# Performance work log

Hardware: AMD Instinct MI355X
Metric: run time of the kernel (lower is better)

## Reference

```python
import jax, jax.numpy as jnp
import numpy as np


def setup_inputs() -> dict:
    key = jax.random.key(0)
    k1, k2 = jax.random.split(key)
    B, S_ENC, S_DEC, D = 8, 2048, 2048, 1024
    enc_outputs = jax.random.normal(k1, (B, S_ENC, D), dtype=jnp.float32)
    dec_outputs = jax.random.normal(k2, (B, S_DEC, D), dtype=jnp.float32)
    return {"enc_outputs": enc_outputs, "dec_outputs": dec_outputs}


def reference(enc_outputs, dec_outputs):
    # scores: [B, S_enc, S_dec] = enc @ dec^T (unscaled)
    a_t = jnp.einsum('bed,btd->bet', enc_outputs, dec_outputs)
    a_t = jax.nn.softmax(a_t, axis=-1)
    # context: [B, S_dec, D] = a_t^T @ enc
    c_t = jnp.einsum('bet,bed->btd', a_t, enc_outputs)
    return c_t
```

## Files before the change

### kernel.cpp

```cpp
#include <hip/hip_runtime.h>


typedef _Float16 half8 __attribute__((ext_vector_type(8)));
typedef _Float16 half4v __attribute__((ext_vector_type(4)));
typedef float floatx16 __attribute__((ext_vector_type(16)));

#define BM 128
#define BN 128
#define BK 64

__device__ __forceinline__ void async_load16(const _Float16* g, void* l) {
  __builtin_amdgcn_global_load_lds(
      (const __attribute__((address_space(1))) void*)g,
      (__attribute__((address_space(3))) void*)l, 16, 0, 0);
}

template <typename OutT, bool TRANS, int RN>
__global__ __launch_bounds__(256, 2) void gemm_bt(
    const _Float16* __restrict__ A, const _Float16* __restrict__ Bt,
    OutT* __restrict__ C, int K, long strideA, long strideB, long strideC,
    int ldA, int ldB, int ldC) {
  constexpr int CPR = BK / 8;
  constexpr int SK = BK / 16;
  __shared__ alignas(16) char smem[TRANS ? (128 * 136 * 2) : (2 * BM * BK * 2)];
  _Float16* lds_a = (_Float16*)smem;
  _Float16* lds_b = (_Float16*)(smem + BM * BK * 2);

  const int b = blockIdx.z;
  A += (long)b * strideA;
  Bt += (long)b * strideB;
  C += (long)b * strideC;

  const int id = blockIdx.y * gridDim.x + blockIdx.x;
  const int xcd = id & 7;
  const int l = id >> 3;
  const int m0 = ((xcd & 3) * 4 + l / RN) * BM;
  const int n0 = ((xcd >> 2) * RN + l % RN) * BN;

  const int tid = threadIdx.x;
  const int lane = tid & 63;
  const int wave = tid >> 6;
  const int l31 = lane & 31;
  const int kh = lane >> 5;
  const int wm = (wave >> 1) * 64;
  const int wn = (wave & 1) * 64;

  floatx16 acc[2][2] = {};

  for (int k0 = 0; k0 < K; k0 += BK) {
#pragma unroll
    for (int c = 0; c < 4; ++c) {
      const int off = c * 4096 + wave * 1024 + lane * 16;
      const int row = off >> 7;
      const int ke = (((off >> 4) & (CPR - 1)) ^ (row & (CPR - 1))) * 8;
      async_load16(A + (long)(m0 + row) * ldA + k0 + ke, (char*)lds_a + off);
      async_load16(Bt + (long)(n0 + row) * ldB + k0 + ke, (char*)lds_b + off);
    }
    __syncthreads();

    half8 af[2][SK], bf[2][SK];
#pragma unroll
    for (int i = 0; i < 2; ++i) {
      const int ra = wm + i * 32 + l31;
      const int rb = wn + i * 32 + l31;
#pragma unroll
      for (int s = 0; s < SK; ++s) {
        const int ck = s * 2 + kh;
        af[i][s] = *(const half8*)((const char*)lds_a + ra * (BK * 2) +
                                   ((ck ^ (ra & (CPR - 1))) << 4));
        bf[i][s] = *(const half8*)((const char*)lds_b + rb * (BK * 2) +
                                   ((ck ^ (rb & (CPR - 1))) << 4));
      }
    }
#pragma unroll
    for (int s = 0; s < SK; ++s)
#pragma unroll
      for (int i = 0; i < 2; ++i)
#pragma unroll
        for (int j = 0; j < 2; ++j)
          acc[i][j] = __builtin_amdgcn_mfma_f32_32x32x16_f16(
              af[i][s], bf[j][s], acc[i][j], 0, 0, 0);
    __syncthreads();
  }

  if constexpr (TRANS) {
    _Float16(*TT)[136] = (_Float16(*)[136])smem;
#pragma unroll
    for (int i = 0; i < 2; ++i)
#pragma unroll
      for (int j = 0; j < 2; ++j) {
        const int tl = wn + j * 32 + l31;
#pragma unroll
        for (int g = 0; g < 4; ++g) {
          half4v h;
#pragma unroll
          for (int rr = 0; rr < 4; ++rr) h[rr] = (_Float16)acc[i][j][g * 4 + rr];
          *(half4v*)&TT[tl][wm + i * 32 + 4 * kh + g * 8] = h;
        }
      }
    __syncthreads();
#pragma unroll
    for (int p = 0; p < 8; ++p) {
      const int idx = p * 256 + tid;
      const int tl = idx >> 4;
      const int ck = idx & 15;
      *(half8*)((_Float16*)C + (long)(n0 + tl) * ldC + m0 + ck * 8) =
          *(const half8*)&TT[tl][ck * 8];
    }
  } else {
#pragma unroll
    for (int i = 0; i < 2; ++i) {
      const int r_base = m0 + wm + i * 32 + 4 * kh;
#pragma unroll
      for (int j = 0; j < 2; ++j) {
        const int col = n0 + wn + j * 32 + l31;
#pragma unroll
        for (int g = 0; g < 4; ++g)
#pragma unroll
          for (int rr = 0; rr < 4; ++rr)
            C[(long)(r_base + g * 8 + rr) * ldC + col] =
                (OutT)acc[i][j][g * 4 + rr];
      }
    }
  }
}

__global__ __launch_bounds__(256) void conv_enc(const float* __restrict__ E,
                                                _Float16* __restrict__ Eh,
                                                _Float16* __restrict__ EhT,
                                                int Se, int D) {
  __shared__ _Float16 T[64][72];
  const int b = blockIdx.z;
  const int d0 = blockIdx.x * 64;
  const int e0 = blockIdx.y * 64;
  const float* Eb = E + (size_t)b * Se * D;
  _Float16* Ehb = Eh + (size_t)b * Se * D;
  _Float16* EhTb = EhT + (size_t)b * D * Se;
  const int tid = threadIdx.x;
  const int tx = tid & 15;
  const int ty = tid >> 4;

  half4v h[4];
#pragma unroll
  for (int r = 0; r < 4; ++r) {
    const int e = e0 + ty * 4 + r;
    float4 v = *(const float4*)(Eb + (size_t)e * D + d0 + tx * 4);
    h[r][0] = (_Float16)v.x; h[r][1] = (_Float16)v.y;
    h[r][2] = (_Float16)v.z; h[r][3] = (_Float16)v.w;
    *(half4v*)(Ehb + (size_t)e * D + d0 + tx * 4) = h[r];
  }
#pragma unroll
  for (int c = 0; c < 4; ++c) {
    half4v w;
#pragma unroll
    for (int r = 0; r < 4; ++r) w[r] = h[r][c];
    *(half4v*)&T[tx * 4 + c][ty * 4] = w;
  }
  __syncthreads();
#pragma unroll
  for (int p = 0; p < 2; ++p) {
    const int idx = tid + p * 256;
    const int row = idx >> 3;
    const int ck = idx & 7;
    *(half8*)(EhTb + (size_t)(d0 + row) * Se + e0 + ck * 8) =
        *(const half8*)&T[row][ck * 8];
  }
}

__global__ __launch_bounds__(256) void conv_dec(const float* __restrict__ X,
                                                _Float16* __restrict__ Y) {
  const size_t i = ((size_t)blockIdx.x * 256 + threadIdx.x) * 8;
  float4 a = *(const float4*)(X + i);
  float4 b = *(const float4*)(X + i + 4);
  half8 h;
  h[0] = (_Float16)a.x; h[1] = (_Float16)a.y;
  h[2] = (_Float16)a.z; h[3] = (_Float16)a.w;
  h[4] = (_Float16)b.x; h[5] = (_Float16)b.y;
  h[6] = (_Float16)b.z; h[7] = (_Float16)b.w;
  *(half8*)(Y + i) = h;
}

__global__ __launch_bounds__(256) void col_stats(const _Float16* __restrict__ ST,
                                                 float2* __restrict__ part) {
  __shared__ float2 red[16][65];
  const int b = blockIdx.z;
  const int e0 = blockIdx.x * 64;
  const int t0 = blockIdx.y * 512;
  const _Float16* S = ST + (size_t)b * 2048 * 2048;
  const int tx = threadIdx.x & 15;
  const int ty = threadIdx.x >> 4;

  float m[4] = {-1e30f, -1e30f, -1e30f, -1e30f};
  float s[4] = {0.f, 0.f, 0.f, 0.f};
  for (int it = 0; it < 32; ++it) {
    const int t = t0 + it * 16 + ty;
    half4v v = *(const half4v*)(S + (size_t)t * 2048 + e0 + tx * 4);
#pragma unroll
    for (int c = 0; c < 4; ++c) {
      const float x = (float)v[c];
      const float m2 = fmaxf(m[c], x);
      s[c] = s[c] * __expf(m[c] - m2) + __expf(x - m2);
      m[c] = m2;
    }
  }
#pragma unroll
  for (int c = 0; c < 4; ++c) red[ty][tx * 4 + c] = make_float2(m[c], s[c]);
  __syncthreads();
  if (threadIdx.x < 64) {
    float2 a = red[0][threadIdx.x];
#pragma unroll
    for (int r = 1; r < 16; ++r) {
      const float2 o = red[r][threadIdx.x];
      const float m2 = fmaxf(a.x, o.x);
      a.y = a.y * __expf(a.x - m2) + o.y * __expf(o.x - m2);
      a.x = m2;
    }
    part[(size_t)blockIdx.y * 16384 + (size_t)b * 2048 + e0 + threadIdx.x] = a;
  }
}

__global__ __launch_bounds__(256) void stats_combine(
    const float2* __restrict__ part, float2* __restrict__ stats) {
  const int idx = blockIdx.x * 256 + threadIdx.x;
  float2 a = part[idx];
#pragma unroll
  for (int tc = 1; tc < 4; ++tc) {
    const float2 o = part[tc * 16384 + idx];
    const float m2 = fmaxf(a.x, o.x);
    a.y = a.y * __expf(a.x - m2) + o.y * __expf(o.x - m2);
    a.x = m2;
  }
  stats[idx] = make_float2(a.x, 1.0f / a.y);
}

__global__ __launch_bounds__(256) void norm_stream(
    const _Float16* __restrict__ ST, const float2* __restrict__ stats,
    _Float16* __restrict__ P) {
  const int b = blockIdx.y;
  const int t0 = blockIdx.x * 4;
  const int e = threadIdx.x * 8;
  float m_[8], rl_[8];
#pragma unroll
  for (int j = 0; j < 8; ++j) {
    const float2 st = stats[(size_t)b * 2048 + e + j];
    m_[j] = st.x;
    rl_[j] = st.y;
  }
  const size_t base = ((size_t)b * 2048 + t0) * 2048 + e;
#pragma unroll
  for (int r = 0; r < 4; ++r) {
    half8 v = *(const half8*)(ST + base + (size_t)r * 2048);
    half8 o;
#pragma unroll
    for (int j = 0; j < 8; ++j)
      o[j] = (_Float16)(__expf((float)v[j] - m_[j]) * rl_[j]);
    *(half8*)(P + base + (size_t)r * 2048) = o;
  }
}

extern "C" void kernel_launch(void* const* d_in, const int* in_sizes, int n_in,
                              void* d_out, int out_size, void* d_ws,
                              size_t ws_size, hipStream_t stream) {
  const float* enc = (const float*)d_in[0];
  const float* dec = (const float*)d_in[1];
  float* out = (float*)d_out;

  const int B = 8, SE = 2048, SD = 2048, D = 1024;
  char* ws = (char*)d_ws;
  _Float16* enc_h = (_Float16*)ws;
  _Float16* dec_h = (_Float16*)(ws + 33554432);
  _Float16* P = (_Float16*)ws;
  _Float16* enc_hT = (_Float16*)(ws + 67108864);
  _Float16* ST = (_Float16*)(ws + 100663296);
  float2* stats = (float2*)(ws + 167772160);
  float2* part = (float2*)(ws + 167903232);

  conv_enc<<<dim3(D / 64, SE / 64, B), 256, 0, stream>>>(enc, enc_h, enc_hT,
                                                         SE, D);
  conv_dec<<<dim3((size_t)B * SD * D / 2048), 256, 0, stream>>>(dec, dec_h);
  gemm_bt<_Float16, true, 8><<<dim3(SD / BN, SE / BM, B), 256, 0, stream>>>(
      enc_h, dec_h, ST, D, (long)SE * D, (long)SD * D, (long)SE * SD, D, D,
      SE);
  col_stats<<<dim3(32, 4, B), 256, 0, stream>>>(ST, part);
  stats_combine<<<dim3(64), 256, 0, stream>>>(part, stats);
  norm_stream<<<dim3(512, B), 256, 0, stream>>>(ST, stats, P);
  gemm_bt<float, false, 4><<<dim3(D / BN, SD / BM, B), 256, 0, stream>>>(
      P, enc_hT, out, SE, (long)SD * SE, (long)D * SE, (long)SD * D, SE, SE,
      D);
}
```

Measured before the change: 364.9 us.

## Replace GEMM with 256x256 double-buffered 8-wave pipelined MFMA kernel

Replaces the 128x128 single-stage GEMM with a 256x256 tile kernel using 512 threads, 128KB of dynamic LDS with double buffering, and 16x16x32 MFMAs interleaved with async global-to-LDS loads. Barriers, priority hints and vmcnt waits are placed by hand. The score GEMM now computes the transposed layout directly by swapping its operands, which drops the LDS transpose epilogue. The aim is to hide load latency and raise arithmetic intensity per tile. In exchange, occupancy falls and the epilogue's stores are scalar and strided.

```diff
diff --git a/kernel.cpp b/kernel.cpp
--- a/kernel.cpp
+++ b/kernel.cpp
@@ -3,11 +3,7 @@
 
 typedef _Float16 half8 __attribute__((ext_vector_type(8)));
 typedef _Float16 half4v __attribute__((ext_vector_type(4)));
-typedef float floatx16 __attribute__((ext_vector_type(16)));
-
-#define BM 128
-#define BN 128
-#define BK 64
+typedef float floatx4 __attribute__((ext_vector_type(4)));
 
 __device__ __forceinline__ void async_load16(const _Float16* g, void* l) {
   __builtin_amdgcn_global_load_lds(
@@ -15,112 +11,150 @@
       (__attribute__((address_space(3))) void*)l, 16, 0, 0);
 }
 
-template <typename OutT, bool TRANS, int RN>
-__global__ __launch_bounds__(256, 2) void gemm_bt(
+template <typename OutT>
+__global__ __launch_bounds__(512, 2) void gemm8p(
     const _Float16* __restrict__ A, const _Float16* __restrict__ Bt,
     OutT* __restrict__ C, int K, long strideA, long strideB, long strideC,
     int ldA, int ldB, int ldC) {
-  constexpr int CPR = BK / 8;
-  constexpr int SK = BK / 16;
-  __shared__ alignas(16) char smem[TRANS ? (128 * 136 * 2) : (2 * BM * BK * 2)];
-  _Float16* lds_a = (_Float16*)smem;
-  _Float16* lds_b = (_Float16*)(smem + BM * BK * 2);
-
-  const int b = blockIdx.z;
-  A += (long)b * strideA;
-  Bt += (long)b * strideB;
-  C += (long)b * strideC;
-
-  const int id = blockIdx.y * gridDim.x + blockIdx.x;
-  const int xcd = id & 7;
-  const int l = id >> 3;
-  const int m0 = ((xcd & 3) * 4 + l / RN) * BM;
-  const int n0 = ((xcd >> 2) * RN + l % RN) * BN;
-
+  extern __shared__ char smem_[];
   const int tid = threadIdx.x;
   const int lane = tid & 63;
   const int wave = tid >> 6;
-  const int l31 = lane & 31;
-  const int kh = lane >> 5;
-  const int wm = (wave >> 1) * 64;
-  const int wn = (wave & 1) * 64;
-
-  floatx16 acc[2][2] = {};
-
-  for (int k0 = 0; k0 < K; k0 += BK) {
-#pragma unroll
-    for (int c = 0; c < 4; ++c) {
-      const int off = c * 4096 + wave * 1024 + lane * 16;
+  const int wm = wave >> 2;
+  const int wn = wave & 3;
+  const int l15 = lane & 15;
+  const int lh = lane >> 4;
+
+  const int gx = gridDim.x, gxy = gridDim.x * gridDim.y;
+  int fid = blockIdx.z * gxy + blockIdx.y * gx + blockIdx.x;
+  const int nwg = gxy * gridDim.z;
+  fid = (fid & 7) * (nwg >> 3) + (fid >> 3);
+  const int b = fid / gxy;
+  const int rem = fid - b * gxy;
+  const int m0 = (rem / gx) * 256;
+  const int n0 = (rem % gx) * 256;
+
+  A += (long)b * strideA + (long)m0 * ldA;
+  Bt += (long)b * strideB + (long)n0 * ldB;
+  C += (long)b * strideC;
+
+  floatx4 acc[8][4] = {};
+  half8 a[4][2], b0[2][2], b1[2][2];
+
+  auto stage = [&](const _Float16* g, int ld, int k0, char* slot) {
+#pragma unroll
+    for (int i = 0; i < 4; ++i) {
+      const int off = i * 8192 + tid * 16;
       const int row = off >> 7;
-      const int ke = (((off >> 4) & (CPR - 1)) ^ (row & (CPR - 1))) * 8;
-      async_load16(A + (long)(m0 + row) * ldA + k0 + ke, (char*)lds_a + off);
-      async_load16(Bt + (long)(n0 + row) * ldB + k0 + ke, (char*)lds_b + off);
+      const int ck = (off >> 4) & 7;
+      async_load16(g + (long)row * ld + k0 + ((ck ^ (row & 7)) << 3),
+                   slot + off);
     }
-    __syncthreads();
-
-    half8 af[2][SK], bf[2][SK];
-#pragma unroll
-    for (int i = 0; i < 2; ++i) {
-      const int ra = wm + i * 32 + l31;
-      const int rb = wn + i * 32 + l31;
-#pragma unroll
-      for (int s = 0; s < SK; ++s) {
-        const int ck = s * 2 + kh;
-        af[i][s] = *(const half8*)((const char*)lds_a + ra * (BK * 2) +
-                                   ((ck ^ (ra & (CPR - 1))) << 4));
-        bf[i][s] = *(const half8*)((const char*)lds_b + rb * (BK * 2) +
-                                   ((ck ^ (rb & (CPR - 1))) << 4));
-      }
-    }
-#pragma unroll
-    for (int s = 0; s < SK; ++s)
-#pragma unroll
-      for (int i = 0; i < 2; ++i)
-#pragma unroll
-        for (int j = 0; j < 2; ++j)
-          acc[i][j] = __builtin_amdgcn_mfma_f32_32x32x16_f16(
-              af[i][s], bf[j][s], acc[i][j], 0, 0, 0);
-    __syncthreads();
-  }
-
-  if constexpr (TRANS) {
-    _Float16(*TT)[136] = (_Float16(*)[136])smem;
-#pragma unroll
-    for (int i = 0; i < 2; ++i)
-#pragma unroll
-      for (int j = 0; j < 2; ++j) {
-        const int tl = wn + j * 32 + l31;
-#pragma unroll
-        for (int g = 0; g < 4; ++g) {
-          half4v h;
-#pragma unroll
-          for (int rr = 0; rr < 4; ++rr) h[rr] = (_Float16)acc[i][j][g * 4 + rr];
-          *(half4v*)&TT[tl][wm + i * 32 + 4 * kh + g * 8] = h;
-        }
-      }
-    __syncthreads();
-#pragma unroll
-    for (int p = 0; p < 8; ++p) {
-      const int idx = p * 256 + tid;
-      const int tl = idx >> 4;
-      const int ck = idx & 15;
-      *(half8*)((_Float16*)C + (long)(n0 + tl) * ldC + m0 + ck * 8) =
-          *(const half8*)&TT[tl][ck * 8];
-    }
-  } else {
-#pragma unroll
-    for (int i = 0; i < 2; ++i) {
-      const int r_base = m0 + wm + i * 32 + 4 * kh;
-#pragma unroll
-      for (int j = 0; j < 2; ++j) {
-        const int col = n0 + wn + j * 32 + l31;
-#pragma unroll
-        for (int g = 0; g < 4; ++g)
-#pragma unroll
-          for (int rr = 0; rr < 4; ++rr)
-            C[(long)(r_base + g * 8 + rr) * ldC + col] =
-                (OutT)acc[i][j][g * 4 + rr];
-      }
+  };
+  auto ldf = [&](const char* slot, int row, int s) -> half8 {
+    const int ck = (s * 4 + lh) ^ (row & 7);
+    return *(const half8*)(slot + row * 128 + ck * 16);
+  };
+  auto mm = [&](int mh, int nh, half8(&bb)[2][2]) {
+#pragma unroll
+    for (int s = 0; s < 2; ++s)
+#pragma unroll
+      for (int q = 0; q < 4; ++q)
+#pragma unroll
+        for (int n = 0; n < 2; ++n)
+          acc[mh * 4 + q][nh * 2 + n] = __builtin_amdgcn_mfma_f32_16x16x32_f16(
+              a[q][s], bb[n][s], acc[mh * 4 + q][nh * 2 + n], 0, 0, 0);
+  };
+  auto barrier_ = [&]() {
+    __builtin_amdgcn_sched_barrier(0);
+    asm volatile("" ::: "memory");
+    __builtin_amdgcn_s_barrier();
+    asm volatile("" ::: "memory");
+    __builtin_amdgcn_sched_barrier(0);
+  };
+  auto lgkm0_ = [&]() {
+    asm volatile("s_waitcnt lgkmcnt(0)" ::: "memory");
+    __builtin_amdgcn_sched_barrier(0);
+  };
+
+  auto quad4 = [&](int cur, int kst, int vmn) {
+    const char* as_ = smem_ + cur * 32768 + wm * 16384;
+    const char* bs_ = smem_ + 65536 + cur * 32768 + (wn >> 1) * 16384;
+    const int brow = (wn & 1) * 64;
+#pragma unroll
+    for (int q = 0; q < 4; ++q)
+#pragma unroll
+      for (int s = 0; s < 2; ++s) a[q][s] = ldf(as_, q * 16 + l15, s);
+#pragma unroll
+    for (int n = 0; n < 2; ++n)
+#pragma unroll
+      for (int s = 0; s < 2; ++s) b0[n][s] = ldf(bs_, brow + n * 16 + l15, s);
+    barrier_();
+    lgkm0_();
+    __builtin_amdgcn_s_setprio(1);
+    mm(0, 0, b0);
+    __builtin_amdgcn_s_setprio(0);
+    barrier_();
+#pragma unroll
+    for (int n = 0; n < 2; ++n)
+#pragma unroll
+      for (int s = 0; s < 2; ++s)
+        b1[n][s] = ldf(bs_, brow + (n + 2) * 16 + l15, s);
+    barrier_();
+    lgkm0_();
+    __builtin_amdgcn_s_setprio(1);
+    mm(0, 1, b1);
+    __builtin_amdgcn_s_setprio(0);
+    barrier_();
+#pragma unroll
+    for (int q = 0; q < 4; ++q)
+#pragma unroll
+      for (int s = 0; s < 2; ++s) a[q][s] = ldf(as_, (q + 4) * 16 + l15, s);
+    if (kst >= 0) stage(Bt, ldB, kst, smem_ + 65536 + cur * 32768);
+    barrier_();
+    lgkm0_();
+    __builtin_amdgcn_s_setprio(1);
+    mm(1, 1, b1);
+    __builtin_amdgcn_s_setprio(0);
+    barrier_();
+    if (kst >= 0) stage(A, ldA, kst, smem_ + cur * 32768);
+    barrier_();
+    lgkm0_();
+    __builtin_amdgcn_s_setprio(1);
+    mm(1, 0, b0);
+    __builtin_amdgcn_s_setprio(0);
+    if (vmn)
+      asm volatile("s_waitcnt vmcnt(8)" ::: "memory");
+    else
+      asm volatile("s_waitcnt vmcnt(0)" ::: "memory");
+    __builtin_amdgcn_sched_barrier(0);
+    barrier_();
+  };
+
+  stage(A, ldA, 0, smem_);
+  stage(Bt, ldB, 0, smem_ + 65536);
+  stage(A, ldA, 64, smem_ + 32768);
+  stage(Bt, ldB, 64, smem_ + 65536 + 32768);
+  asm volatile("s_waitcnt vmcnt(8)" ::: "memory");
+  barrier_();
+
+  const int NT = K >> 6;
+  for (int i = 0; i < (NT >> 1) - 1; ++i) {
+    quad4(0, (2 * i + 2) * 64, 1);
+    quad4(1, (2 * i + 3) * 64, 1);
+  }
+  quad4(0, -1, 0);
+  quad4(1, -1, 0);
+
+#pragma unroll
+  for (int mf = 0; mf < 8; ++mf) {
+    const long r0 = (long)(m0 + wm * 128 + mf * 16 + lh * 4);
+#pragma unroll
+    for (int nf = 0; nf < 4; ++nf) {
+      const int cc = n0 + wn * 64 + nf * 16 + l15;
+#pragma unroll
+      for (int rr = 0; rr < 4; ++rr)
+        C[(r0 + rr) * ldC + cc] = (OutT)acc[mf][nf][rr];
     }
   }
 }
@@ -275,16 +309,27 @@
   float2* stats = (float2*)(ws + 167772160);
   float2* part = (float2*)(ws + 167903232);
 
+  static int smem_set = 0;
+  if (!smem_set) {
+    (void)hipFuncSetAttribute(
+        reinterpret_cast<const void*>(&gemm8p<_Float16>),
+        hipFuncAttributeMaxDynamicSharedMemorySize, 131072);
+    (void)hipFuncSetAttribute(
+        reinterpret_cast<const void*>(&gemm8p<float>),
+        hipFuncAttributeMaxDynamicSharedMemorySize, 131072);
+    smem_set = 1;
+  }
+
   conv_enc<<<dim3(D / 64, SE / 64, B), 256, 0, stream>>>(enc, enc_h, enc_hT,
                                                          SE, D);
   conv_dec<<<dim3((size_t)B * SD * D / 2048), 256, 0, stream>>>(dec, dec_h);
-  gemm_bt<_Float16, true, 8><<<dim3(SD / BN, SE / BM, B), 256, 0, stream>>>(
-      enc_h, dec_h, ST, D, (long)SE * D, (long)SD * D, (long)SE * SD, D, D,
+  gemm8p<_Float16><<<dim3(SE / 256, SD / 256, B), 512, 131072, stream>>>(
+      dec_h, enc_h, ST, D, (long)SD * D, (long)SE * D, (long)SD * SE, D, D,
       SE);
   col_stats<<<dim3(32, 4, B), 256, 0, stream>>>(ST, part);
   stats_combine<<<dim3(64), 256, 0, stream>>>(part, stats);
   norm_stream<<<dim3(512, B), 256, 0, stream>>>(ST, stats, P);
-  gemm_bt<float, false, 4><<<dim3(D / BN, SD / BM, B), 256, 0, stream>>>(
+  gemm8p<float><<<dim3(D / 256, SD / 256, B), 512, 131072, stream>>>(
       P, enc_hT, out, SE, (long)SD * SE, (long)D * SE, (long)SD * D, SE, SE,
       D);
 }
```

Result: faster. 334.9 us (-8.2%).
